# Optimization experiments

Hardware: AMD Instinct MI355X
Metric: run time of the kernel (lower is better)

The kernel has to match this reference:

```python
import jax, jax.numpy as jnp
import numpy as np

EMBED = 1024
HEADS = 16
HEAD_DIM = EMBED // HEADS
SEQ = 2048
BATCH = 2


def setup_inputs() -> dict:
    key = jax.random.key(0)
    ks = jax.random.split(key, 5)
    s = 1.0 / np.sqrt(EMBED)
    return {
        "x": jax.random.normal(ks[0], (BATCH, SEQ, EMBED), jnp.float32),
        "W_qkv": jax.random.uniform(ks[1], (EMBED, 3 * EMBED), jnp.float32, -s, s),
        "b_qkv": jax.random.uniform(ks[2], (3 * EMBED,), jnp.float32, -s, s),
        "W_out": jax.random.uniform(ks[3], (EMBED, EMBED), jnp.float32, -s, s),
        "b_out": jax.random.uniform(ks[4], (EMBED,), jnp.float32, -s, s),
    }


def reference(x, W_qkv, b_qkv, W_out, b_out):
    B, S, E = x.shape
    qkv = x @ W_qkv + b_qkv                      # [B,S,3E]
    q, k, v = jnp.split(qkv, 3, axis=-1)
    # [B,S,E] -> [B,H,S,D]
    def heads(t):
        return t.reshape(B, S, HEADS, HEAD_DIM).transpose(0, 2, 1, 3)
    q, k, v = heads(q), heads(k), heads(v)
    scores = jnp.einsum("bhid,bhjd->bhij", q, k) / np.sqrt(HEAD_DIM)  # [B,H,S,S]
    causal = jnp.tril(jnp.ones((S, S), bool))
    scores = jnp.where(causal[None, None], scores, -jnp.inf)
    probs = jax.nn.softmax(scores, axis=-1)
    out = jnp.einsum("bhij,bhjd->bhid", probs, v)  # [B,H,S,D]
    out = out.transpose(0, 2, 1, 3).reshape(B, S, E)
    return out @ W_out + b_out
```

## Files before the change

### kernel.cpp

```cpp
#include <hip/hip_runtime.h>
#include <hip/hip_bf16.h>
#include <cstdint>
#include <cstddef>


typedef unsigned short u16;
typedef __attribute__((ext_vector_type(8))) short short8;
typedef __attribute__((ext_vector_type(4))) short short4v;
typedef __attribute__((ext_vector_type(4))) float floatx4;

#define MFMA16(a, b, c) __builtin_amdgcn_mfma_f32_16x16x32_bf16((a), (b), (c), 0, 0, 0)

#if __has_builtin(__builtin_amdgcn_mfma_f32_16x16x16_bf16)
#define PV_MFMA(a, b, c) __builtin_amdgcn_mfma_f32_16x16x16_bf16((a), (b), (c), 0, 0, 0)
#elif __has_builtin(__builtin_amdgcn_mfma_f32_16x16x16bf16_1k)
#define PV_MFMA(a, b, c) __builtin_amdgcn_mfma_f32_16x16x16bf16_1k((a), (b), (c), 0, 0, 0)
#else
static __device__ __forceinline__ floatx4 pv_mfma_asm(short4v a, short4v b, floatx4 c) {
    asm volatile("v_mfma_f32_16x16x16_bf16 %0, %1, %2, %0" : "+v"(c) : "v"(a), "v"(b));
    return c;
}
#define PV_MFMA(a, b, c) pv_mfma_asm((a), (b), (c))
#endif

#if __has_builtin(__builtin_amdgcn_exp2f)
#define EXP2(x) __builtin_amdgcn_exp2f(x)
#else
#define EXP2(x) exp2f(x)
#endif

#define QSCALE 0.18033688011f
#define NEGINF (-__builtin_inff())

static __device__ __forceinline__ u16 f2b(float f) {
    union { float f; uint32_t u; } v; v.f = f;
    return (u16)((v.u + 0x7fffu + ((v.u >> 16) & 1u)) >> 16);
}

static __device__ __forceinline__ uint32_t pkbf(float lo, float hi) {
    union { float f; uint32_t u; } a, b; a.f = lo; b.f = hi;
    return __builtin_amdgcn_perm(b.u + 0x8000u, a.u + 0x8000u, 0x07060302u);
}

static __device__ __forceinline__ void async_cp16(const u16* g, u16* lds_wave_base) {
    __builtin_amdgcn_global_load_lds((__attribute__((address_space(1))) void*)g,
                                     (__attribute__((address_space(3))) void*)lds_wave_base,
                                     16, 0, 0);
}


__global__ __launch_bounds__(256) void k_prep(const float* __restrict__ x,
                                              const float* __restrict__ Wq,
                                              const float* __restrict__ Wo,
                                              u16* __restrict__ xb,
                                              u16* __restrict__ wqkvT,
                                              u16* __restrict__ woutT) {
    int bx = blockIdx.x, tid = threadIdx.x;
    if (bx < 2048) {
        int g = bx * 256 + tid;
        const float4* s = (const float4*)x + (size_t)g * 2;
        float4 f0 = s[0], f1 = s[1];
        uint4 r;
        r.x = pkbf(f0.x, f0.y);
        r.y = pkbf(f0.z, f0.w);
        r.z = pkbf(f1.x, f1.y);
        r.w = pkbf(f1.z, f1.w);
        *(uint4*)(xb + (size_t)g * 8) = r;
        return;
    }
    __shared__ float t[32][33];
    const float* src;
    u16* dst;
    int R, C, b;
    if (bx < 5120) { b = bx - 2048; src = Wq; dst = wqkvT; R = 1024; C = 3072; }
    else           { b = bx - 5120; src = Wo; dst = woutT; R = 1024; C = 1024; }
    int nbx = C >> 5;
    int yq = b / nbx, xq = b - yq * nbx;
    int c0 = xq * 32, r0 = yq * 32;
    int tx = tid & 31, ty = tid >> 5;
#pragma unroll
    for (int i = 0; i < 4; ++i)
        t[ty + i * 8][tx] = src[(size_t)(r0 + ty + i * 8) * C + c0 + tx];
    __syncthreads();
#pragma unroll
    for (int i = 0; i < 4; ++i)
        dst[(size_t)(c0 + ty + i * 8) * R + r0 + tx] = f2b(t[tx][ty + i * 8]);
}


__global__ __launch_bounds__(256, 3) void k_qkv_gemm(const u16* __restrict__ A,
                                                     const u16* __restrict__ Bt,
                                                     const float* __restrict__ bias,
                                                     u16* __restrict__ Qb,
                                                     u16* __restrict__ Kb,
                                                     u16* __restrict__ Vtb) {
    __shared__ __align__(16) u16 As[3][128 * 32];
    __shared__ __align__(16) u16 Bs[3][128 * 32];
    int tid = threadIdx.x;
    int w = tid >> 6, lane = tid & 63, quad = lane >> 4, l16 = lane & 15;
    int wm = w >> 1, wn = w & 1;
    int m0 = blockIdx.y * 128, n0 = blockIdx.x * 128;
    int wb = (tid & ~63) * 8;

    int ra0 = tid >> 2, ca0 = (tid & 3) * 8;
    int ra1 = (256 + tid) >> 2, ca1 = (tid & 3) * 8;
    const u16* A0 = &A[(size_t)(m0 + ra0) * 1024 + ca0];
    const u16* A1 = &A[(size_t)(m0 + ra1) * 1024 + ca1];
    const u16* B0 = &Bt[(size_t)(n0 + ra0) * 1024 + ca0];
    const u16* B1 = &Bt[(size_t)(n0 + ra1) * 1024 + ca1];

    auto stage = [&](int src_kt, int slot) {
        int ko = src_kt * 32;
        async_cp16(A0 + ko, &As[slot][wb]);
        async_cp16(A1 + ko, &As[slot][2048 + wb]);
        async_cp16(B0 + ko, &Bs[slot][wb]);
        async_cp16(B1 + ko, &Bs[slot][2048 + wb]);
    };

    floatx4 acc[4][4] = {};
    stage(0, 0);
    stage(1, 1);

    for (int kt = 0; kt < 32; ++kt) {
        asm volatile("s_waitcnt vmcnt(4)" ::: "memory");
        asm volatile("s_barrier" ::: "memory");
        int jn = kt + 2;
        stage(jn < 32 ? jn : 31, jn % 3);
        int s = kt % 3;
        short8 af[4], bf[4];
#pragma unroll
        for (int mt = 0; mt < 4; ++mt)
            af[mt] = *(const short8*)&As[s][(wm * 64 + mt * 16 + l16) * 32 + quad * 8];
#pragma unroll
        for (int nt = 0; nt < 4; ++nt)
            bf[nt] = *(const short8*)&Bs[s][(wn * 64 + nt * 16 + l16) * 32 + quad * 8];
#pragma unroll
        for (int mt = 0; mt < 4; ++mt)
#pragma unroll
            for (int nt = 0; nt < 4; ++nt)
                acc[mt][nt] = MFMA16(af[mt], bf[nt], acc[mt][nt]);
    }

    int region = n0 >> 10;
    if (region == 2) {
#pragma unroll
        for (int mt = 0; mt < 4; ++mt)
#pragma unroll
            for (int nt = 0; nt < 4; ++nt) {
                int n_abs = n0 + wn * 64 + nt * 16 + l16;
                int e = n_abs & 1023, h = e >> 6, d = e & 63;
                float vb = bias[n_abs];
                int mrow = m0 + wm * 64 + mt * 16 + quad * 4;
                int b = mrow >> 11, s0 = mrow & 2047;
                uint2 val;
                val.x = pkbf(acc[mt][nt][0] + vb, acc[mt][nt][1] + vb);
                val.y = pkbf(acc[mt][nt][2] + vb, acc[mt][nt][3] + vb);
                *(uint2*)&Vtb[((size_t)(b * 16 + h) * 64 + d) * 2048 + s0] = val;
            }
    } else {
        u16* dst = region == 0 ? Qb : Kb;
        float scl = region == 0 ? QSCALE : 1.0f;
#pragma unroll
        for (int mt = 0; mt < 4; ++mt)
#pragma unroll
            for (int nt = 0; nt < 4; ++nt)
#pragma unroll
                for (int r = 0; r < 4; ++r) {
                    int m_abs = m0 + wm * 64 + mt * 16 + quad * 4 + r;
                    int n_abs = n0 + wn * 64 + nt * 16 + l16;
                    float val = (acc[mt][nt][r] + bias[n_abs]) * scl;
                    int e = n_abs & 1023, h = e >> 6, d = e & 63;
                    int b = m_abs >> 11, s = m_abs & 2047;
                    dst[((size_t)(b * 16 + h) * 2048 + s) * 64 + d] = f2b(val);
                }
    }
}


__global__ __launch_bounds__(256, 4) void k_out_gemm(const u16* __restrict__ A,
                                                     const u16* __restrict__ Bt,
                                                     const float* __restrict__ bias,
                                                     float* __restrict__ out) {
    __shared__ __align__(16) u16 As[3][64 * 32];
    __shared__ __align__(16) u16 Bs[3][128 * 32];
    int tid = threadIdx.x;
    int w = tid >> 6, lane = tid & 63, quad = lane >> 4, l16 = lane & 15;
    int wm = w >> 1, wn = w & 1;
    int m0 = blockIdx.y * 64, n0 = blockIdx.x * 128;
    int wb = (tid & ~63) * 8;

    int ra0 = tid >> 2, ca0 = (tid & 3) * 8;
    int ra1 = (256 + tid) >> 2;
    const u16* A0 = &A[(size_t)(m0 + ra0) * 1024 + ca0];
    const u16* B0 = &Bt[(size_t)(n0 + ra0) * 1024 + ca0];
    const u16* B1 = &Bt[(size_t)(n0 + ra1) * 1024 + ca0];

    auto stage = [&](int src_kt, int slot) {
        int ko = src_kt * 32;
        async_cp16(A0 + ko, &As[slot][wb]);
        async_cp16(B0 + ko, &Bs[slot][wb]);
        async_cp16(B1 + ko, &Bs[slot][2048 + wb]);
    };

    floatx4 acc[2][4] = {};
    stage(0, 0);
    stage(1, 1);

    for (int kt = 0; kt < 32; ++kt) {
        asm volatile("s_waitcnt vmcnt(3)" ::: "memory");
        asm volatile("s_barrier" ::: "memory");
        int jn = kt + 2;
        stage(jn < 32 ? jn : 31, jn % 3);
        int s = kt % 3;
        short8 af[2], bf[4];
#pragma unroll
        for (int mt = 0; mt < 2; ++mt)
            af[mt] = *(const short8*)&As[s][(wm * 32 + mt * 16 + l16) * 32 + quad * 8];
#pragma unroll
        for (int nt = 0; nt < 4; ++nt)
            bf[nt] = *(const short8*)&Bs[s][(wn * 64 + nt * 16 + l16) * 32 + quad * 8];
#pragma unroll
        for (int mt = 0; mt < 2; ++mt)
#pragma unroll
            for (int nt = 0; nt < 4; ++nt)
                acc[mt][nt] = MFMA16(af[mt], bf[nt], acc[mt][nt]);
    }

#pragma unroll
    for (int mt = 0; mt < 2; ++mt)
#pragma unroll
        for (int nt = 0; nt < 4; ++nt)
#pragma unroll
            for (int r = 0; r < 4; ++r) {
                int m_abs = m0 + wm * 32 + mt * 16 + quad * 4 + r;
                int n_abs = n0 + wn * 64 + nt * 16 + l16;
                out[(size_t)m_abs * 1024 + n_abs] = acc[mt][nt][r] + bias[n_abs];
            }
}


__global__ __launch_bounds__(512, 4) void k_attn(const u16* __restrict__ Qb,
                                                 const u16* __restrict__ Kb,
                                                 const u16* __restrict__ Vtb,
                                                 u16* __restrict__ attnb) {
    __shared__ __align__(16) u16 KV[4][2][4096];
    int tid = threadIdx.x;
    int w = tid >> 6, lane = tid & 63, quad = lane >> 4, l16 = lane & 15;
    int L = blockIdx.x;
    int bh = ((L & 7) << 2) | ((L >> 3) & 3);
    int idx = (L >> 5) & 15;
    int tile = idx < 8 ? idx : 23 - idx;
    const u16* Qp = Qb + (size_t)bh * 131072;
    const u16* Kp = Kb + (size_t)bh * 131072;
    const u16* Vp = Vtb + (size_t)bh * 131072;
    int b = bh >> 4, h = bh & 15;

    int r0 = tid >> 3, c0 = ((tid & 7) ^ (r0 & 7)) * 8;
    int kOff = r0 * 64 + c0;
    int vOff = r0 * 2048 + c0;
    int wb = (tid & ~63) * 8;

    int strip = w >> 2;
    int q_s = tile * 128 + strip * 64 + (w & 3) * 16 + l16;
    short8 q0 = *(const short8*)&Qp[(size_t)q_s * 64 + quad * 8];
    short8 q1 = *(const short8*)&Qp[(size_t)q_s * 64 + 32 + quad * 8];

    int n = 2 * tile + 2;
    int lastk = n - 2 + strip;

    auto stage = [&](int j) {
        u16* Ks = (u16*)KV[j & 3][0];
        u16* Vs = (u16*)KV[j & 3][1];
        async_cp16(Kp + (size_t)j * 4096 + kOff, Ks + wb);
        async_cp16(Vp + (size_t)j * 64 + vOff, Vs + wb);
    };

    floatx4 acc[4] = {};
    float lp = 0.f;
    int sw = l16 & 7;

    stage(0); stage(1); stage(2);

    for (int kt = 0; kt < n; ++kt) {
        asm volatile("s_waitcnt vmcnt(4)" ::: "memory");
        asm volatile("s_barrier" ::: "memory");
        {
            int jn = kt + 3;
            stage(jn < n ? jn : n - 1);
        }
        if (kt <= lastk) {
            const u16* Ks = (const u16*)KV[kt & 3][0];
            const u16* Vs = (const u16*)KV[kt & 3][1];

            short8 kfa[4], kfb[4];
#pragma unroll
            for (int nt = 0; nt < 4; ++nt) {
                int rb = (nt * 16 + l16) * 8;
                kfa[nt] = *(const short8*)&Ks[(rb + (quad ^ sw)) * 8];
                kfb[nt] = *(const short8*)&Ks[(rb + ((4 + quad) ^ sw)) * 8];
            }
            short4v vf[4][4];
#pragma unroll
            for (int dt = 0; dt < 4; ++dt) {
                const char* rowb = (const char*)Vs + (dt * 16 + l16) * 128 + (quad & 1) * 8;
#pragma unroll
                for (int nt = 0; nt < 4; ++nt) {
                    int chunk = nt * 2 + (quad >> 1);
                    vf[nt][dt] = *(const short4v*)(rowb + ((chunk ^ sw) * 16));
                }
            }

            floatx4 sa[4] = {};
#pragma unroll
            for (int nt = 0; nt < 4; ++nt) {
                sa[nt] = MFMA16(kfa[nt], q0, sa[nt]);
                sa[nt] = MFMA16(kfb[nt], q1, sa[nt]);
            }
            if (kt == lastk) {
#pragma unroll
                for (int nt = 0; nt < 4; ++nt)
#pragma unroll
                    for (int r = 0; r < 4; ++r)
                        if (kt * 64 + nt * 16 + quad * 4 + r > q_s)
                            sa[nt][r] = NEGINF;
            }
            float p[4][4];
#pragma unroll
            for (int nt = 0; nt < 4; ++nt)
#pragma unroll
                for (int r = 0; r < 4; ++r)
                    p[nt][r] = EXP2(sa[nt][r]);
            float s0 = (p[0][0] + p[0][1]) + (p[0][2] + p[0][3]);
            float s1 = (p[1][0] + p[1][1]) + (p[1][2] + p[1][3]);
            float s2 = (p[2][0] + p[2][1]) + (p[2][2] + p[2][3]);
            float s3 = (p[3][0] + p[3][1]) + (p[3][2] + p[3][3]);
            lp += (s0 + s1) + (s2 + s3);
#pragma unroll
            for (int nt = 0; nt < 4; ++nt) {
                union { uint2 u; short4v s; } pf;
                pf.u.x = pkbf(p[nt][0], p[nt][1]);
                pf.u.y = pkbf(p[nt][2], p[nt][3]);
#pragma unroll
                for (int dt = 0; dt < 4; ++dt)
                    acc[dt] = PV_MFMA(vf[nt][dt], pf.s, acc[dt]);
            }
        }
    }

    float lr = lp;
    lr += __shfl_xor(lr, 16);
    lr += __shfl_xor(lr, 32);
    float inv = 1.f / lr;
    size_t base = ((size_t)(b * 2048 + q_s)) * 1024 + h * 64;
#pragma unroll
    for (int dt = 0; dt < 4; ++dt) {
        uint2 val;
        val.x = pkbf(acc[dt][0] * inv, acc[dt][1] * inv);
        val.y = pkbf(acc[dt][2] * inv, acc[dt][3] * inv);
        *(uint2*)&attnb[base + dt * 16 + quad * 4] = val;
    }
}


extern "C" void kernel_launch(void* const* d_in, const int* in_sizes, int n_in,
                              void* d_out, int out_size, void* d_ws, size_t ws_size,
                              hipStream_t stream) {
    const float* x     = (const float*)d_in[0];
    const float* W_qkv = (const float*)d_in[1];
    const float* b_qkv = (const float*)d_in[2];
    const float* W_out = (const float*)d_in[3];
    const float* b_out = (const float*)d_in[4];
    float* out = (float*)d_out;

    char* p = (char*)d_ws;
    u16* xb    = (u16*)p; p += (size_t)4096 * 1024 * 2;
    u16* wqkvT = (u16*)p; p += (size_t)3072 * 1024 * 2;
    u16* woutT = (u16*)p; p += (size_t)1024 * 1024 * 2;
    u16* Qb    = (u16*)p; p += (size_t)32 * 2048 * 64 * 2;
    u16* Kb    = (u16*)p; p += (size_t)32 * 2048 * 64 * 2;
    u16* Vtb   = (u16*)p; p += (size_t)32 * 64 * 2048 * 2;
    u16* attnb = xb;

    k_prep<<<6144, 256, 0, stream>>>(x, W_qkv, W_out, xb, wqkvT, woutT);
    k_qkv_gemm<<<dim3(24, 32), 256, 0, stream>>>(xb, wqkvT, b_qkv, Qb, Kb, Vtb);
    k_attn<<<512, 512, 0, stream>>>(Qb, Kb, Vtb, attnb);
    k_out_gemm<<<dim3(8, 64), 256, 0, stream>>>(attnb, woutT, b_out, out);
}
```

Measured before the change: 173.0 us.

## Split key tiles across warp groups and merge partial attention outputs in LDS

The attention kernel now has each warp handle 32 query rows, with its two 16-row blocks sharing K/V fragments. The two warp groups each process half of every 64-key tile instead of one 64-row strip each. This halves per-warp K/V LDS fragment loads per query and balances causal work between groups, which previously differed by one tile. Partial accumulators and row sums are combined through shared memory at the end, adding a sync and a scratch pass. MFMA sections are also wrapped with s_setprio to favour matrix issue.

Result: no change. 173.9 us (+0.6%).

```diff
diff --git a/kernel.cpp b/kernel.cpp
--- a/kernel.cpp
+++ b/kernel.cpp
@@ -260,13 +260,17 @@
     int vOff = r0 * 2048 + c0;
     int wb = (tid & ~63) * 8;
 
-    int strip = w >> 2;
-    int q_s = tile * 128 + strip * 64 + (w & 3) * 16 + l16;
-    short8 q0 = *(const short8*)&Qp[(size_t)q_s * 64 + quad * 8];
-    short8 q1 = *(const short8*)&Qp[(size_t)q_s * 64 + 32 + quad * 8];
+    int g  = w >> 2;
+    int wq = w & 3;
+    int q_a = tile * 128 + wq * 32 + l16;
+    int q_b = q_a + 16;
+    short8 qa0 = *(const short8*)&Qp[(size_t)q_a * 64 + quad * 8];
+    short8 qa1 = *(const short8*)&Qp[(size_t)q_a * 64 + 32 + quad * 8];
+    short8 qb0 = *(const short8*)&Qp[(size_t)q_b * 64 + quad * 8];
+    short8 qb1 = *(const short8*)&Qp[(size_t)q_b * 64 + 32 + quad * 8];
 
     int n = 2 * tile + 2;
-    int lastk = n - 2 + strip;
+    int lastk = 2 * tile + (wq >> 1);
 
     auto stage = [&](int j) {
         u16* Ks = (u16*)KV[j & 3][0];
@@ -275,8 +279,8 @@
         async_cp16(Vp + (size_t)j * 64 + vOff, Vs + wb);
     };
 
-    floatx4 acc[4] = {};
-    float lp = 0.f;
+    floatx4 acc[2][4] = {};
+    float lp[2] = {0.f, 0.f};
     int sw = l16 & 7;
 
     stage(0); stage(1); stage(2);
@@ -292,72 +296,115 @@
             const u16* Ks = (const u16*)KV[kt & 3][0];
             const u16* Vs = (const u16*)KV[kt & 3][1];
 
-            short8 kfa[4], kfb[4];
-#pragma unroll
-            for (int nt = 0; nt < 4; ++nt) {
-                int rb = (nt * 16 + l16) * 8;
+            short8 kfa[2], kfb[2];
+#pragma unroll
+            for (int nt = 0; nt < 2; ++nt) {
+                int rb = (g * 32 + nt * 16 + l16) * 8;
                 kfa[nt] = *(const short8*)&Ks[(rb + (quad ^ sw)) * 8];
                 kfb[nt] = *(const short8*)&Ks[(rb + ((4 + quad) ^ sw)) * 8];
             }
-            short4v vf[4][4];
+            short4v vf[2][4];
 #pragma unroll
             for (int dt = 0; dt < 4; ++dt) {
                 const char* rowb = (const char*)Vs + (dt * 16 + l16) * 128 + (quad & 1) * 8;
 #pragma unroll
-                for (int nt = 0; nt < 4; ++nt) {
-                    int chunk = nt * 2 + (quad >> 1);
+                for (int nt = 0; nt < 2; ++nt) {
+                    int chunk = g * 4 + nt * 2 + (quad >> 1);
                     vf[nt][dt] = *(const short4v*)(rowb + ((chunk ^ sw) * 16));
                 }
             }
 
-            floatx4 sa[4] = {};
-#pragma unroll
-            for (int nt = 0; nt < 4; ++nt) {
-                sa[nt] = MFMA16(kfa[nt], q0, sa[nt]);
-                sa[nt] = MFMA16(kfb[nt], q1, sa[nt]);
-            }
+            floatx4 sa[2][2] = {};
+            __builtin_amdgcn_s_setprio(1);
+#pragma unroll
+            for (int nt = 0; nt < 2; ++nt) {
+                sa[0][nt] = MFMA16(kfa[nt], qa0, sa[0][nt]);
+                sa[0][nt] = MFMA16(kfb[nt], qa1, sa[0][nt]);
+                sa[1][nt] = MFMA16(kfa[nt], qb0, sa[1][nt]);
+                sa[1][nt] = MFMA16(kfb[nt], qb1, sa[1][nt]);
+            }
+            __builtin_amdgcn_s_setprio(0);
             if (kt == lastk) {
 #pragma unroll
-                for (int nt = 0; nt < 4; ++nt)
+                for (int nt = 0; nt < 2; ++nt)
+#pragma unroll
+                    for (int r = 0; r < 4; ++r) {
+                        int key = kt * 64 + g * 32 + nt * 16 + quad * 4 + r;
+                        if (key > q_a) sa[0][nt][r] = NEGINF;
+                        if (key > q_b) sa[1][nt][r] = NEGINF;
+                    }
+            }
+            float p[2][2][4];
+#pragma unroll
+            for (int rb = 0; rb < 2; ++rb)
+#pragma unroll
+                for (int nt = 0; nt < 2; ++nt)
 #pragma unroll
                     for (int r = 0; r < 4; ++r)
-                        if (kt * 64 + nt * 16 + quad * 4 + r > q_s)
-                            sa[nt][r] = NEGINF;
-            }
-            float p[4][4];
-#pragma unroll
-            for (int nt = 0; nt < 4; ++nt)
-#pragma unroll
-                for (int r = 0; r < 4; ++r)
-                    p[nt][r] = EXP2(sa[nt][r]);
-            float s0 = (p[0][0] + p[0][1]) + (p[0][2] + p[0][3]);
-            float s1 = (p[1][0] + p[1][1]) + (p[1][2] + p[1][3]);
-            float s2 = (p[2][0] + p[2][1]) + (p[2][2] + p[2][3]);
-            float s3 = (p[3][0] + p[3][1]) + (p[3][2] + p[3][3]);
-            lp += (s0 + s1) + (s2 + s3);
-#pragma unroll
-            for (int nt = 0; nt < 4; ++nt) {
-                union { uint2 u; short4v s; } pf;
-                pf.u.x = pkbf(p[nt][0], p[nt][1]);
-                pf.u.y = pkbf(p[nt][2], p[nt][3]);
-#pragma unroll
-                for (int dt = 0; dt < 4; ++dt)
-                    acc[dt] = PV_MFMA(vf[nt][dt], pf.s, acc[dt]);
-            }
+                        p[rb][nt][r] = EXP2(sa[rb][nt][r]);
+#pragma unroll
+            for (int rb = 0; rb < 2; ++rb) {
+                float s0 = (p[rb][0][0] + p[rb][0][1]) + (p[rb][0][2] + p[rb][0][3]);
+                float s1 = (p[rb][1][0] + p[rb][1][1]) + (p[rb][1][2] + p[rb][1][3]);
+                lp[rb] += s0 + s1;
+            }
+            union { uint2 u; short4v s; } pf[2][2];
+#pragma unroll
+            for (int rb = 0; rb < 2; ++rb)
+#pragma unroll
+                for (int nt = 0; nt < 2; ++nt) {
+                    pf[rb][nt].u.x = pkbf(p[rb][nt][0], p[rb][nt][1]);
+                    pf[rb][nt].u.y = pkbf(p[rb][nt][2], p[rb][nt][3]);
+                }
+            __builtin_amdgcn_s_setprio(1);
+#pragma unroll
+            for (int rb = 0; rb < 2; ++rb)
+#pragma unroll
+                for (int nt = 0; nt < 2; ++nt)
+#pragma unroll
+                    for (int dt = 0; dt < 4; ++dt)
+                        acc[rb][dt] = PV_MFMA(vf[nt][dt], pf[rb][nt].s, acc[rb][dt]);
+            __builtin_amdgcn_s_setprio(0);
         }
     }
 
-    float lr = lp;
-    lr += __shfl_xor(lr, 16);
-    lr += __shfl_xor(lr, 32);
-    float inv = 1.f / lr;
-    size_t base = ((size_t)(b * 2048 + q_s)) * 1024 + h * 64;
-#pragma unroll
-    for (int dt = 0; dt < 4; ++dt) {
-        uint2 val;
-        val.x = pkbf(acc[dt][0] * inv, acc[dt][1] * inv);
-        val.y = pkbf(acc[dt][2] * inv, acc[dt][3] * inv);
-        *(uint2*)&attnb[base + dt * 16 + quad * 4] = val;
+    asm volatile("s_waitcnt vmcnt(0)" ::: "memory");
+    __syncthreads();
+    float* scr  = (float*)KV;
+    float* lscr = scr + 128 * 64;
+    if (g == 1) {
+#pragma unroll
+        for (int rb = 0; rb < 2; ++rb) {
+            int ql = wq * 32 + rb * 16 + l16;
+#pragma unroll
+            for (int dt = 0; dt < 4; ++dt)
+                *(floatx4*)&scr[ql * 64 + dt * 16 + quad * 4] = acc[rb][dt];
+            float lr1 = lp[rb];
+            lr1 += __shfl_xor(lr1, 16);
+            lr1 += __shfl_xor(lr1, 32);
+            lscr[ql] = lr1;
+        }
+    }
+    __syncthreads();
+    if (g == 0) {
+#pragma unroll
+        for (int rb = 0; rb < 2; ++rb) {
+            int ql = wq * 32 + rb * 16 + l16;
+            float lr = lp[rb];
+            lr += __shfl_xor(lr, 16);
+            lr += __shfl_xor(lr, 32);
+            lr += lscr[ql];
+            float inv = 1.f / lr;
+            size_t base = ((size_t)(b * 2048 + tile * 128 + ql)) * 1024 + h * 64;
+#pragma unroll
+            for (int dt = 0; dt < 4; ++dt) {
+                floatx4 o = acc[rb][dt] + *(const floatx4*)&scr[ql * 64 + dt * 16 + quad * 4];
+                uint2 val;
+                val.x = pkbf(o[0] * inv, o[1] * inv);
+                val.y = pkbf(o[2] * inv, o[3] * inv);
+                *(uint2*)&attnb[base + dt * 16 + quad * 4] = val;
+            }
+        }
     }
 }
 
```

## Stage 128-key tiles with double buffering instead of 64-key quad buffering

Applied to the files above, without the earlier changes.

The attention kernel now loads K/V in 128-key chunks into two shared buffers rather than 64-key chunks into four. It waits for all outstanding loads (vmcnt(0)) and prefetches only one tile ahead, while each iteration processes two 64-key halves with per-warp causal early exit. This halves the number of barriers and loop iterations. In exchange the prefetch distance shrinks, so load latency is less hidden, and the causal skip is now done per warp inside the larger tile.

Result: no change. 170.8 us (-1.3%).

```diff
diff --git a/kernel.cpp b/kernel.cpp
--- a/kernel.cpp
+++ b/kernel.cpp
@@ -243,7 +243,7 @@
                                                  const u16* __restrict__ Kb,
                                                  const u16* __restrict__ Vtb,
                                                  u16* __restrict__ attnb) {
-    __shared__ __align__(16) u16 KV[4][2][4096];
+    __shared__ __align__(16) u16 KV[2][2][8192];
     int tid = threadIdx.x;
     int w = tid >> 6, lane = tid & 63, quad = lane >> 4, l16 = lane & 15;
     int L = blockIdx.x;
@@ -255,58 +255,67 @@
     const u16* Vp = Vtb + (size_t)bh * 131072;
     int b = bh >> 4, h = bh & 15;
 
-    int r0 = tid >> 3, c0 = ((tid & 7) ^ (r0 & 7)) * 8;
-    int kOff = r0 * 64 + c0;
-    int vOff = r0 * 2048 + c0;
+    int rk = tid >> 3;
+    int ck = ((tid & 7) ^ (rk & 7)) * 8;
+    int kOff = rk * 64 + ck;
+    int rv = tid >> 4;
+    int cv = tid & 15;
+    int gvc = (cv & 8) | ((cv & 7) ^ (rv & 7));
+    int vOff = rv * 2048 + gvc * 8;
     int wb = (tid & ~63) * 8;
 
     int strip = w >> 2;
-    int q_s = tile * 128 + strip * 64 + (w & 3) * 16 + l16;
+    int Q0 = tile * 128 + strip * 64 + (w & 3) * 16;
+    int q_s = Q0 + l16;
     short8 q0 = *(const short8*)&Qp[(size_t)q_s * 64 + quad * 8];
     short8 q1 = *(const short8*)&Qp[(size_t)q_s * 64 + 32 + quad * 8];
 
-    int n = 2 * tile + 2;
-    int lastk = n - 2 + strip;
+    int n = tile + 1;
 
     auto stage = [&](int j) {
-        u16* Ks = (u16*)KV[j & 3][0];
-        u16* Vs = (u16*)KV[j & 3][1];
-        async_cp16(Kp + (size_t)j * 4096 + kOff, Ks + wb);
-        async_cp16(Vp + (size_t)j * 64 + vOff, Vs + wb);
+        u16* Ks = (u16*)KV[j & 1][0];
+        u16* Vs = (u16*)KV[j & 1][1];
+        const u16* kp = Kp + (size_t)j * 8192;
+        const u16* vp = Vp + (size_t)j * 128;
+        async_cp16(kp + kOff, Ks + wb);
+        async_cp16(kp + kOff + 4096, Ks + 4096 + wb);
+        async_cp16(vp + vOff, Vs + wb);
+        async_cp16(vp + vOff + 65536, Vs + 4096 + wb);
     };
 
     floatx4 acc[4] = {};
     float lp = 0.f;
     int sw = l16 & 7;
 
-    stage(0); stage(1); stage(2);
+    stage(0);
 
     for (int kt = 0; kt < n; ++kt) {
-        asm volatile("s_waitcnt vmcnt(4)" ::: "memory");
+        asm volatile("s_waitcnt vmcnt(0)" ::: "memory");
         asm volatile("s_barrier" ::: "memory");
-        {
-            int jn = kt + 3;
-            stage(jn < n ? jn : n - 1);
-        }
-        if (kt <= lastk) {
-            const u16* Ks = (const u16*)KV[kt & 3][0];
-            const u16* Vs = (const u16*)KV[kt & 3][1];
+        if (kt + 1 < n) stage(kt + 1);
+        const u16* Ks = (const u16*)KV[kt & 1][0];
+        const u16* Vs = (const u16*)KV[kt & 1][1];
+
+#pragma unroll
+        for (int hh = 0; hh < 2; ++hh) {
+            int kb = kt * 128 + hh * 64;
+            if (kb > Q0) break;
 
             short8 kfa[4], kfb[4];
 #pragma unroll
             for (int nt = 0; nt < 4; ++nt) {
-                int rb = (nt * 16 + l16) * 8;
+                int rb = (hh * 64 + nt * 16 + l16) * 8;
                 kfa[nt] = *(const short8*)&Ks[(rb + (quad ^ sw)) * 8];
                 kfb[nt] = *(const short8*)&Ks[(rb + ((4 + quad) ^ sw)) * 8];
             }
             short4v vf[4][4];
 #pragma unroll
             for (int dt = 0; dt < 4; ++dt) {
-                const char* rowb = (const char*)Vs + (dt * 16 + l16) * 128 + (quad & 1) * 8;
+                const char* rowb = (const char*)Vs + (dt * 16 + l16) * 256 + (quad & 1) * 8;
 #pragma unroll
                 for (int nt = 0; nt < 4; ++nt) {
-                    int chunk = nt * 2 + (quad >> 1);
-                    vf[nt][dt] = *(const short4v*)(rowb + ((chunk ^ sw) * 16));
+                    int chunk = hh * 8 + ((nt * 2 + (quad >> 1)) ^ sw);
+                    vf[nt][dt] = *(const short4v*)(rowb + chunk * 16);
                 }
             }
 
@@ -316,12 +325,12 @@
                 sa[nt] = MFMA16(kfa[nt], q0, sa[nt]);
                 sa[nt] = MFMA16(kfb[nt], q1, sa[nt]);
             }
-            if (kt == lastk) {
+            if (kb + 63 > Q0) {
 #pragma unroll
                 for (int nt = 0; nt < 4; ++nt)
 #pragma unroll
                     for (int r = 0; r < 4; ++r)
-                        if (kt * 64 + nt * 16 + quad * 4 + r > q_s)
+                        if (kb + nt * 16 + quad * 4 + r > q_s)
                             sa[nt][r] = NEGINF;
             }
             float p[4][4];
```
